# Kernel optimization log

Measured on AMD Instinct MI355X. Metric: run time of the kernel, lower is better.

## Reference

```python
import jax, jax.numpy as jnp
import numpy as np
from jax import lax

K = 16  # knn_k


def _mlp(x, W1, b1, W2, b2):
    h = jax.nn.gelu(x @ W1 + b1, approximate=False)  # torch nn.GELU default = exact
    return h @ W2 + b2


def setup_inputs() -> dict:
    key = jax.random.key(0)
    ks = jax.random.split(key, 10)
    B, N, F, H = 8, 4096, 64, 128

    def xav(k, shape):
        fan_in = shape[0]
        return (jax.random.normal(k, shape, jnp.float32) / np.sqrt(fan_in)).astype(jnp.float32)

    return {
        "coords": jax.random.normal(ks[0], (B, N, 3), jnp.float32),
        "features": jax.random.normal(ks[1], (B, N, F), jnp.float32),
        "inv_W1": xav(ks[2], (6, H)), "inv_b1": jnp.zeros((H,), jnp.float32),
        "inv_W2": xav(ks[3], (H, H)), "inv_b2": jnp.zeros((H,), jnp.float32),
        "feat_W1": xav(ks[4], (F, H)), "feat_b1": jnp.zeros((H,), jnp.float32),
        "feat_W2": xav(ks[5], (H, H)), "feat_b2": jnp.zeros((H,), jnp.float32),
        "sh_W1": xav(ks[6], (2 * H, H)), "sh_b1": jnp.zeros((H,), jnp.float32),
        "sh_W2": xav(ks[7], (H, H)), "sh_b2": jnp.zeros((H,), jnp.float32),
        "g0_W": xav(ks[8], (H, 1)), "g0_b": jnp.zeros((1,), jnp.float32),
    }


def _local_geometry(coords):
    # coords: [B,N,3]
    B, N, _ = coords.shape
    k = min(K, N - 1)
    # squared pairwise distances (monotone in euclidean dist -> same kNN indices)
    sq = jnp.sum(coords * coords, axis=-1)                    # [B,N]
    dist2 = sq[:, :, None] + sq[:, None, :] - 2.0 * jnp.einsum("bnd,bmd->bnm", coords, coords)
    dist2 = lax.stop_gradient(dist2)
    eye = jnp.eye(N, dtype=bool)
    dist2 = jnp.where(eye[None], jnp.inf, dist2)
    _, idx = lax.top_k(-dist2, k)                             # smallest-k -> [B,N,k]
    neighbors = jax.vmap(lambda c, i: c[i])(coords, idx)      # [B,N,k,3]
    relative = neighbors - coords[:, :, None, :]              # [B,N,k,3]
    cov = jnp.einsum("bnki,bnkj->bnij", relative, relative) / float(k)  # [B,N,3,3]
    evals, evecs = jnp.linalg.eigh(cov)                       # ascending
    normals = evecs[..., 0]                                   # smallest-eigval eigenvector, [B,N,3]
    center = coords.mean(axis=1, keepdims=True)
    outward = coords - center
    orient = jnp.sign(jnp.sum(normals * outward, axis=-1, keepdims=True))
    orient = jnp.where(orient == 0, 1.0, orient)
    normals = normals * orient
    normals = normals / jnp.maximum(jnp.linalg.norm(normals, axis=-1, keepdims=True), 1e-6)
    radius = jnp.linalg.norm(relative, axis=-1).mean(axis=-1, keepdims=True)   # [B,N,1]
    centered_radius = jnp.linalg.norm(outward, axis=-1, keepdims=True)
    eig_sum = jnp.maximum(evals.sum(axis=-1, keepdims=True), 1e-6)
    dominance = evals[..., 2:3] / eig_sum
    invariants = jnp.concatenate([evals, radius, centered_radius, dominance], axis=-1)  # [B,N,6]
    return normals, invariants


def reference(coords, features, inv_W1, inv_b1, inv_W2, inv_b2,
              feat_W1, feat_b1, feat_W2, feat_b2,
              sh_W1, sh_b1, sh_W2, sh_b2, g0_W, g0_b):
    normals, invariants = _local_geometry(coords)
    inv_h = _mlp(invariants, inv_W1, inv_b1, inv_W2, inv_b2)
    feat_h = _mlp(features, feat_W1, feat_b1, feat_W2, feat_b2)
    hidden = _mlp(jnp.concatenate([inv_h, feat_h], axis=-1), sh_W1, sh_b1, sh_W2, sh_b2)
    scalar = hidden @ g0_W + g0_b                                   # grade 0, [B,N,1]
    plane = jnp.stack([normals[..., 0], normals[..., 1], -normals[..., 2],
                       -jnp.sum(coords * normals, axis=-1)], axis=-1)  # grade 1, [B,N,4]
    biv = jnp.concatenate([normals, jnp.zeros_like(normals)], axis=-1)  # grade 2, [B,N,6]
    point = jnp.concatenate([coords, jnp.ones(coords.shape[:-1] + (1,), coords.dtype)], axis=-1)  # grade 3 OPNS point
    zero4 = jnp.zeros(coords.shape[:-1] + (1,), coords.dtype)            # grade 4
    return jnp.concatenate([scalar, plane, biv, point, zero4], axis=-1)  # [B,N,16]
```

## Files before the change

kernel.cpp:

```cpp
#include <hip/hip_runtime.h>
#include <hip/hip_bf16.h>

#define BB 8
#define NN 4096
#define FF 64
#define HH 128
#define KNN 16

typedef __attribute__((ext_vector_type(8))) short bf16x8;
typedef __attribute__((ext_vector_type(4))) short bf16x4;
typedef __attribute__((ext_vector_type(4))) float f32x4;

#define OFF_iW2 0
#define OFF_fW1 16384
#define OFF_fW2 24576
#define OFF_sW1 40960
#define OFF_sW2 73728
#define HI_SZ   90112

__device__ __forceinline__ float sq3(float x, float y, float z) {
    return fmaf(z, z, fmaf(y, y, __fmul_rn(x, x)));
}
__device__ __forceinline__ float dist2f(float px, float py, float pz, float psq, float4 cc) {
    float t = fmaf(pz, cc.z, fmaf(py, cc.y, __fmul_rn(px, cc.x)));
    return __fsub_rn(__fadd_rn(psq, cc.w), __fmul_rn(2.0f, t));
}

__device__ __forceinline__ short f2bf(float x) {
    unsigned u = __float_as_uint(x);
    u += 0x7fffu + ((u >> 16) & 1u);
    return (short)(u >> 16);
}
__device__ __forceinline__ float bf2f(short s) {
    return __uint_as_float(((unsigned)(unsigned short)s) << 16);
}

extern "C" __global__ __launch_bounds__(256)
void k_prep(const float* __restrict__ coords, float4* __restrict__ coords4, float* __restrict__ center,
            const float* __restrict__ iW2, const float* __restrict__ fW1,
            const float* __restrict__ fW2, const float* __restrict__ sW1,
            const float* __restrict__ sW2, short* __restrict__ wbf) {
    const int bx = blockIdx.x, tid = threadIdx.x;
    __shared__ float rx[256], ry[256], rz[256];
    if (bx < 8) {
        const int b = bx;
        float sx = 0.f, sy = 0.f, sz = 0.f;
        for (int n = tid; n < NN; n += 256) {
            const float* c = coords + (size_t)(b * NN + n) * 3;
            float x = c[0], y = c[1], z = c[2];
            coords4[b * NN + n] = make_float4(x, y, z, sq3(x, y, z));
            sx += x; sy += y; sz += z;
        }
        rx[tid] = sx; ry[tid] = sy; rz[tid] = sz;
        __syncthreads();
        for (int s = 128; s > 0; s >>= 1) {
            if (tid < s) { rx[tid] += rx[tid + s]; ry[tid] += ry[tid + s]; rz[tid] += rz[tid + s]; }
            __syncthreads();
        }
        if (tid == 0) {
            center[b * 4 + 0] = rx[0] * (1.0f / NN);
            center[b * 4 + 1] = ry[0] * (1.0f / NN);
            center[b * 4 + 2] = rz[0] * (1.0f / NN);
        }
    } else {
        const int wb = bx - 8;
        const int w = wb >> 4;
        const int xb = wb & 15;
        const float* W; int K; int off;
        if (w == 0)      { W = iW2; K = 128; off = OFF_iW2; }
        else if (w == 1) { W = fW1; K = 64;  off = OFF_fW1; }
        else if (w == 2) { W = fW2; K = 128; off = OFF_fW2; }
        else if (w == 3) { W = sW1; K = 256; off = OFF_sW1; }
        else             { W = sW2; K = 128; off = OFF_sW2; }
        short* hi = wbf + off;
        short* lo = wbf + HI_SZ + off;
        const int total = K * 128;
        for (int e = xb * 256 + tid; e < total; e += 4096) {
            int j = e & 7, lane = (e >> 3) & 63, ct = (e >> 9) & 7, kb = e >> 12;
            int k = kb * 32 + (lane >> 4) * 8 + j;
            int n = ct * 16 + (lane & 15);
            float v = W[k * 128 + n];
            short h = f2bf(v);
            float r = v - bf2f(h);
            hi[e] = h; lo[e] = f2bf(r);
        }
    }
}

#define JROT(app, aqq, apq, arp, arq, vp0, vp1, vp2, vq0, vq1, vq2) { \
    float tau_ = (aqq - app) / (2.0f * apq); \
    float tt_ = copysignf(1.0f, tau_) / (fabsf(tau_) + sqrtf(1.0f + tau_ * tau_)); \
    if (apq == 0.0f) tt_ = 0.0f; \
    float cc_ = 1.0f / sqrtf(1.0f + tt_ * tt_); \
    float ss_ = tt_ * cc_; \
    float app_n = cc_*cc_*app - 2.0f*cc_*ss_*apq + ss_*ss_*aqq; \
    float aqq_n = ss_*ss_*app + 2.0f*cc_*ss_*apq + cc_*cc_*aqq; \
    float apq_n = cc_*ss_*(app - aqq) + (cc_*cc_ - ss_*ss_)*apq; \
    float arp_n = cc_*arp - ss_*arq; \
    float arq_n = ss_*arp + cc_*arq; \
    app = app_n; aqq = aqq_n; apq = apq_n; arp = arp_n; arq = arq_n; \
    float t0_ = cc_*vp0 - ss_*vq0, t1_ = cc_*vp1 - ss_*vq1, t2_ = cc_*vp2 - ss_*vq2; \
    vq0 = ss_*vp0 + cc_*vq0; vq1 = ss_*vp1 + cc_*vq1; vq2 = ss_*vp2 + cc_*vq2; \
    vp0 = t0_; vp1 = t1_; vp2 = t2_; }

#define SWAPF(a, b) { float sw_ = a; a = b; b = sw_; }

__device__ __forceinline__ void sort16(float (&d)[16]) {
#pragma unroll
    for (int k = 2; k <= 16; k <<= 1) {
#pragma unroll
        for (int j = k >> 1; j > 0; j >>= 1) {
#pragma unroll
            for (int i = 0; i < 16; i++) {
                int l = i ^ j;
                if (l > i) {
                    if ((i & k) == 0) {
                        float mn = fminf(d[i], d[l]);
                        d[l] = fmaxf(d[i], d[l]);
                        d[i] = mn;
                    } else {
                        float mx = fmaxf(d[i], d[l]);
                        d[l] = fminf(d[i], d[l]);
                        d[i] = mx;
                    }
                }
            }
        }
    }
}

__device__ __forceinline__ void merge16(float (&dk)[16], const float (&d)[16]) {
    float t[16];
#pragma unroll
    for (int i = 0; i < 16; i++) t[i] = fminf(dk[i], d[15 - i]);
#pragma unroll
    for (int j = 8; j > 0; j >>= 1) {
#pragma unroll
        for (int i = 0; i < 16; i++) {
            int l = i ^ j;
            if (l > i) {
                float mn = fminf(t[i], t[l]);
                t[l] = fmaxf(t[i], t[l]);
                t[i] = mn;
            }
        }
    }
#pragma unroll
    for (int i = 0; i < 16; i++) dk[i] = t[i];
}

__device__ __forceinline__ void sort16i(int (&d)[16]) {
#pragma unroll
    for (int k = 2; k <= 16; k <<= 1) {
#pragma unroll
        for (int j = k >> 1; j > 0; j >>= 1) {
#pragma unroll
            for (int i = 0; i < 16; i++) {
                int l = i ^ j;
                if (l > i) {
                    int a = d[i], bq = d[l];
                    int mn = a < bq ? a : bq;
                    int mx = a < bq ? bq : a;
                    if ((i & k) == 0) { d[i] = mn; d[l] = mx; }
                    else              { d[i] = mx; d[l] = mn; }
                }
            }
        }
    }
}

__device__ __forceinline__ float gelu_exact(float x) {
    return 0.5f * x * (1.0f + erff(x * 0.70710678118654752440f));
}

template <int KB, bool INIT>
__device__ __forceinline__ void gemm_mfma(const short* Ab, const short* __restrict__ whi,
                                          const short* __restrict__ wlo,
                                          const float* __restrict__ bias,
                                          int wid, int lane, f32x4 acc[2]) {
    const int m16 = lane & 15, quad = lane >> 4;
    if (INIT) {
        float b0 = bias[wid * 16 + m16];
        acc[0] = (f32x4){b0, b0, b0, b0};
        acc[1] = acc[0];
    }
#pragma unroll 1
    for (int kb = 0; kb < KB; kb++) {
        bf16x8 a0 = *(const bf16x8*)(Ab + m16 * 136 + kb * 32 + quad * 8);
        bf16x8 a1 = *(const bf16x8*)(Ab + (m16 + 16) * 136 + kb * 32 + quad * 8);
        const int off = ((kb * 8 + wid) * 64 + lane) * 8;
        bf16x8 bh = *(const bf16x8*)(whi + off);
        bf16x8 bl = *(const bf16x8*)(wlo + off);
        acc[0] = __builtin_amdgcn_mfma_f32_16x16x32_bf16(a0, bh, acc[0], 0, 0, 0);
        acc[0] = __builtin_amdgcn_mfma_f32_16x16x32_bf16(a0, bl, acc[0], 0, 0, 0);
        acc[1] = __builtin_amdgcn_mfma_f32_16x16x32_bf16(a1, bh, acc[1], 0, 0, 0);
        acc[1] = __builtin_amdgcn_mfma_f32_16x16x32_bf16(a1, bl, acc[1], 0, 0, 0);
    }
}

__device__ __forceinline__ void acc_to_bf(short* dst, f32x4 acc[2], int wid, int lane, bool dogelu) {
    const int m16 = lane & 15, quad = lane >> 4;
#pragma unroll
    for (int mt = 0; mt < 2; mt++)
#pragma unroll
        for (int i = 0; i < 4; i++) {
            float v = acc[mt][i];
            if (dogelu) v = gelu_exact(v);
            dst[(mt * 16 + quad * 4 + i) * 136 + wid * 16 + m16] = f2bf(v);
        }
}

extern "C" __global__ __launch_bounds__(512, 8)
void k_fused(const float4* __restrict__ coords4, const float* __restrict__ center,
             const float* __restrict__ features, const short* __restrict__ wbf,
             const float* __restrict__ iW1, const float* __restrict__ ib1,
             const float* __restrict__ ib2,
             const float* __restrict__ fb1, const float* __restrict__ fb2,
             const float* __restrict__ sb1, const float* __restrict__ sb2,
             const float* __restrict__ gW, const float* __restrict__ gb,
             float* __restrict__ out) {
    const int blk = blockIdx.x;
    const int b = blk >> 7;
    const int chunk = blk & 127;
    const int tid = threadIdx.x;
    const int pid = tid & 31;
    const int h = tid >> 5;
    const int n = chunk * 32 + pid;
    const float4* __restrict__ C = coords4 + b * NN;

    __shared__ __align__(16) char smem[36864];
    float4* tile = (float4*)smem;
    float* mb = (float*)smem;
    unsigned short* slist = (unsigned short*)(smem + 16384);
    unsigned short* tlist = (unsigned short*)(smem + 17408);
    int* cnt_s = (int*)(smem + 17920);
    int* cnt_t = (int*)(smem + 18048);
    float* inv8 = (float*)(smem + 18176);
    float* sc   = (float*)(smem + 19200);
    short* Abf  = (short*)(smem + 19328);
    short* FHbf = (short*)(smem + 28032);

    float4 me = C[n];
    const float px = me.x, py = me.y, pz = me.z, psq = me.w;
    const float INF = __builtin_inff();

    float dk[KNN];
#pragma unroll
    for (int i = 0; i < KNN; i++) dk[i] = INF;

    for (int r = 0; r < 4; r++) {
        __syncthreads();
#pragma unroll
        for (int e = tid; e < 1024; e += 512) {
            int seg = e >> 6, idx = e & 63;
            tile[e] = C[seg * 256 + r * 64 + idx];
        }
        __syncthreads();
        const float4* T = &tile[h * 64];
        const int selfj = n - (h * 256 + r * 64);
#pragma unroll
        for (int bt = 0; bt < 4; bt++) {
            float d[16];
#pragma unroll
            for (int i = 0; i < 16; i++) {
                float4 cc = T[bt * 16 + i];
                float dd = dist2f(px, py, pz, psq, cc);
                d[i] = (bt * 16 + i) == selfj ? INF : dd;
            }
            sort16(d);
            merge16(dk, d);
        }
    }

    {
        float o[16];
#pragma unroll
        for (int i = 0; i < KNN; i++) o[i] = __shfl_xor(dk[i], 32);
        merge16(dk, o);
    }
#pragma unroll
    for (int s = 64; s <= 256; s <<= 1) {
        __syncthreads();
#pragma unroll
        for (int i = 0; i < KNN; i++) mb[tid * 17 + i] = dk[i];
        __syncthreads();
        const int ptn = tid ^ s;
        float o[16];
#pragma unroll
        for (int i = 0; i < KNN; i++) o[i] = mb[ptn * 17 + i];
        merge16(dk, o);
    }
    const float d15 = dk[15];

    __syncthreads();
    if (tid < 32) { cnt_s[tid] = 0; cnt_t[tid] = 0; }

    for (int r = 0; r < 4; r++) {
        __syncthreads();
#pragma unroll
        for (int e = tid; e < 1024; e += 512) {
            int seg = e >> 6, idx = e & 63;
            tile[e] = C[seg * 256 + r * 64 + idx];
        }
        __syncthreads();
        const float4* T = &tile[h * 64];
        const int base = h * 256 + r * 64;
#pragma unroll 4
        for (int j = 0; j < 64; j++) {
            float4 cc = T[j];
            float d = dist2f(px, py, pz, psq, cc);
            int g = base + j;
            if (g != n && d <= d15) {
                if (d < d15) {
                    int pos = atomicAdd(&cnt_s[pid], 1);
                    if (pos < 16) slist[pid * 16 + pos] = (unsigned short)g;
                } else {
                    int pos = atomicAdd(&cnt_t[pid], 1);
                    if (pos < 8) tlist[pid * 8 + pos] = (unsigned short)g;
                }
            }
        }
    }
    __syncthreads();

    if (tid < 32) {
        int ns = cnt_s[tid]; ns = ns > 15 ? 15 : ns;
        int ids[16];
#pragma unroll
        for (int j = 0; j < 16; j++) {
            int tj = j - ns; tj = tj < 0 ? 0 : (tj > 7 ? 7 : tj);
            int sid = (int)slist[tid * 16 + j];
            int tie = (int)tlist[tid * 8 + tj];
            ids[j] = (j < ns) ? sid : tie;
        }
        sort16i(ids);

        float cxx = 0.f, cxy = 0.f, cxz = 0.f, cyy = 0.f, cyz = 0.f, czz = 0.f, radsum = 0.f;
#pragma unroll
        for (int j = 0; j < KNN; j++) {
            float4 cc = C[ids[j]];
            float rx = __fsub_rn(cc.x, px), ry = __fsub_rn(cc.y, py), rz = __fsub_rn(cc.z, pz);
            cxx = __fadd_rn(cxx, __fmul_rn(rx, rx));
            cxy = __fadd_rn(cxy, __fmul_rn(rx, ry));
            cxz = __fadd_rn(cxz, __fmul_rn(rx, rz));
            cyy = __fadd_rn(cyy, __fmul_rn(ry, ry));
            cyz = __fadd_rn(cyz, __fmul_rn(ry, rz));
            czz = __fadd_rn(czz, __fmul_rn(rz, rz));
            float rr = __fadd_rn(__fadd_rn(__fmul_rn(rx, rx), __fmul_rn(ry, ry)), __fmul_rn(rz, rz));
            radsum = __fadd_rn(radsum, sqrtf(rr));
        }
        const float inv_k = 1.0f / KNN;
        float a00 = cxx * inv_k, a01 = cxy * inv_k, a02 = cxz * inv_k;
        float a11 = cyy * inv_k, a12 = cyz * inv_k, a22 = czz * inv_k;

        float V00 = 1.f, V01 = 0.f, V02 = 0.f;
        float V10 = 0.f, V11 = 1.f, V12 = 0.f;
        float V20 = 0.f, V21 = 0.f, V22 = 1.f;
        for (int sweep = 0; sweep < 6; sweep++) {
            JROT(a00, a11, a01, a02, a12, V00, V10, V20, V01, V11, V21);
            JROT(a00, a22, a02, a01, a12, V00, V10, V20, V02, V12, V22);
            JROT(a11, a22, a12, a01, a02, V01, V11, V21, V02, V12, V22);
        }
        float e0 = a00, e1 = a11, e2 = a22;
        float x0 = V00, y0 = V10, z0 = V20;
        float x1 = V01, y1 = V11, z1 = V21;
        float x2 = V02, y2 = V12, z2 = V22;
        if (e0 > e1) { SWAPF(e0, e1); SWAPF(x0, x1); SWAPF(y0, y1); SWAPF(z0, z1); }
        if (e1 > e2) { SWAPF(e1, e2); SWAPF(x1, x2); SWAPF(y1, y2); SWAPF(z1, z2); }
        if (e0 > e1) { SWAPF(e0, e1); SWAPF(x0, x1); SWAPF(y0, y1); SWAPF(z0, z1); }

        float cx = center[b * 4 + 0], cy = center[b * 4 + 1], cz = center[b * 4 + 2];
        float ox = __fsub_rn(px, cx), oy = __fsub_rn(py, cy), oz = __fsub_rn(pz, cz);
        float dt = __fadd_rn(__fadd_rn(__fmul_rn(x0, ox), __fmul_rn(y0, oy)), __fmul_rn(z0, oz));
        float sgn = (dt >= 0.0f) ? 1.0f : -1.0f;
        x0 *= sgn; y0 *= sgn; z0 *= sgn;
        float nrm = sqrtf(__fadd_rn(__fadd_rn(__fmul_rn(x0, x0), __fmul_rn(y0, y0)), __fmul_rn(z0, z0)));
        float den = fmaxf(nrm, 1e-6f);
        x0 = x0 / den; y0 = y0 / den; z0 = z0 / den;

        float radius = radsum * inv_k;
        float crad = sqrtf(__fadd_rn(__fadd_rn(__fmul_rn(ox, ox), __fmul_rn(oy, oy)), __fmul_rn(oz, oz)));
        float esum = fmaxf(__fadd_rn(__fadd_rn(e0, e1), e2), 1e-6f);
        float dom = e2 / esum;

        float* ip = inv8 + tid * 8;
        ip[0] = e0; ip[1] = e1; ip[2] = e2; ip[3] = radius; ip[4] = crad; ip[5] = dom;
        ip[6] = 0.f; ip[7] = 0.f;

        float pd = __fadd_rn(__fadd_rn(__fmul_rn(px, x0), __fmul_rn(py, y0)), __fmul_rn(pz, z0));
        float4* o = (float4*)(out + (size_t)(b * NN + n) * 16);
        o[0] = make_float4(0.0f, x0, y0, -z0);
        o[1] = make_float4(-pd, x0, y0, z0);
        o[2] = make_float4(0.0f, 0.0f, 0.0f, px);
        o[3] = make_float4(py, pz, 1.0f, 0.0f);
        sc[tid] = gb[0];
    }
    __syncthreads();

    const int wid = tid >> 6, lane = tid & 63;
    const short* w_iW2h = wbf + OFF_iW2; const short* w_iW2l = wbf + HI_SZ + OFF_iW2;
    const short* w_fW1h = wbf + OFF_fW1; const short* w_fW1l = wbf + HI_SZ + OFF_fW1;
    const short* w_fW2h = wbf + OFF_fW2; const short* w_fW2l = wbf + HI_SZ + OFF_fW2;
    const short* w_sW1h = wbf + OFF_sW1; const short* w_sW1l = wbf + HI_SZ + OFF_sW1;
    const short* w_sW2h = wbf + OFF_sW2; const short* w_sW2l = wbf + HI_SZ + OFF_sW2;
    f32x4 acc[2];

    {
        int row = tid >> 4, c4 = (tid & 15) * 4;
        const float* s = features + (size_t)(b * NN + chunk * 32 + row) * FF + c4;
        float4 v = *(const float4*)s;
        bf16x4 pk;
        pk[0] = f2bf(v.x); pk[1] = f2bf(v.y); pk[2] = f2bf(v.z); pk[3] = f2bf(v.w);
        *(bf16x4*)(Abf + row * 136 + c4) = pk;
    }
    __syncthreads();

    gemm_mfma<2, true>(Abf, w_fW1h, w_fW1l, fb1, wid, lane, acc);
    __syncthreads();
    acc_to_bf(Abf, acc, wid, lane, true);
    __syncthreads();

    gemm_mfma<4, true>(Abf, w_fW2h, w_fW2l, fb2, wid, lane, acc);
    __syncthreads();
    acc_to_bf(FHbf, acc, wid, lane, false);

    {
        const int cg = tid & 31, pg = tid >> 5;
        const int c0 = cg * 4, p0 = pg * 2;
        float4 bb = *(const float4*)(ib1 + c0);
        float a2[2][4];
#pragma unroll
        for (int i = 0; i < 2; i++) { a2[i][0] = bb.x; a2[i][1] = bb.y; a2[i][2] = bb.z; a2[i][3] = bb.w; }
#pragma unroll
        for (int k = 0; k < 6; k++) {
            float4 w = *(const float4*)(iW1 + k * HH + c0);
#pragma unroll
            for (int i = 0; i < 2; i++) {
                float a = inv8[(p0 + i) * 8 + k];
                a2[i][0] = fmaf(a, w.x, a2[i][0]);
                a2[i][1] = fmaf(a, w.y, a2[i][1]);
                a2[i][2] = fmaf(a, w.z, a2[i][2]);
                a2[i][3] = fmaf(a, w.w, a2[i][3]);
            }
        }
#pragma unroll
        for (int i = 0; i < 2; i++) {
            bf16x4 pk;
            pk[0] = f2bf(gelu_exact(a2[i][0])); pk[1] = f2bf(gelu_exact(a2[i][1]));
            pk[2] = f2bf(gelu_exact(a2[i][2])); pk[3] = f2bf(gelu_exact(a2[i][3]));
            *(bf16x4*)(Abf + (p0 + i) * 136 + c0) = pk;
        }
    }
    __syncthreads();

    gemm_mfma<4, true>(Abf, w_iW2h, w_iW2l, ib2, wid, lane, acc);
    __syncthreads();
    acc_to_bf(Abf, acc, wid, lane, false);
    __syncthreads();

    gemm_mfma<4, true>(Abf, w_sW1h, w_sW1l, sb1, wid, lane, acc);
    gemm_mfma<4, false>(FHbf, w_sW1h + 16384, w_sW1l + 16384, nullptr, wid, lane, acc);
    __syncthreads();
    acc_to_bf(Abf, acc, wid, lane, true);
    __syncthreads();

    gemm_mfma<4, true>(Abf, w_sW2h, w_sW2l, sb2, wid, lane, acc);
    {
        const int m16 = lane & 15, quad = lane >> 4;
        float g = gW[wid * 16 + m16];
#pragma unroll
        for (int mt = 0; mt < 2; mt++)
#pragma unroll
            for (int i = 0; i < 4; i++)
                atomicAdd(&sc[mt * 16 + quad * 4 + i], acc[mt][i] * g);
    }
    __syncthreads();
    if (tid < 32) out[(size_t)(b * NN + chunk * 32 + tid) * 16] = sc[tid];
}

extern "C" void kernel_launch(void* const* d_in, const int* in_sizes, int n_in,
                              void* d_out, int out_size, void* d_ws, size_t ws_size,
                              hipStream_t stream) {
    const float* coords   = (const float*)d_in[0];
    const float* features = (const float*)d_in[1];
    const float* iW1 = (const float*)d_in[2],  * ib1 = (const float*)d_in[3];
    const float* iW2 = (const float*)d_in[4],  * ib2 = (const float*)d_in[5];
    const float* fW1 = (const float*)d_in[6],  * fb1 = (const float*)d_in[7];
    const float* fW2 = (const float*)d_in[8],  * fb2 = (const float*)d_in[9];
    const float* sW1 = (const float*)d_in[10], * sb1 = (const float*)d_in[11];
    const float* sW2 = (const float*)d_in[12], * sb2 = (const float*)d_in[13];
    const float* gW  = (const float*)d_in[14], * gb  = (const float*)d_in[15];
    float* out = (float*)d_out;

    float* ws = (float*)d_ws;
    float4* coords4 = (float4*)ws;
    float* center = ws + BB * NN * 4;
    short* wbf = (short*)((char*)d_ws + 524416);

    hipLaunchKernelGGL(k_prep, dim3(88), dim3(256), 0, stream,
                       coords, coords4, center, iW2, fW1, fW2, sW1, sW2, wbf);
    hipLaunchKernelGGL(k_fused, dim3(1024), dim3(512), 0, stream, coords4, center, features, wbf,
                       iW1, ib1, ib2, fb1, fb2, sb1, sb2, gW, gb, out);
}
```

Measured before the change: 265.7 us.

## Interleave kNN candidate split across lanes, reduce with shuffles, read coords from global

Each point's 16 helper threads now sit in adjacent lanes within a wavefront and take candidates in interleaved order (j*16+h). The cross-thread top-k reduction is then four xor-shuffle merges instead of a cross-wave shared-memory exchange with barriers. Coordinate tiles are no longer staged in LDS; candidates are read directly from global/L2, which shrinks shared memory and removes the per-round barriers. The bitonic sort16 is replaced by an explicit 63-comparator merge-sort network, and merge16 now works in place. The cost is that global coordinate loads now rely on the cache rather than LDS reuse.

```diff
diff --git a/kernel.cpp b/kernel.cpp
--- a/kernel.cpp
+++ b/kernel.cpp
@@ -105,48 +105,49 @@
 
 #define SWAPF(a, b) { float sw_ = a; a = b; b = sw_; }
 
+__device__ __forceinline__ void ce(float& a, float& b) {
+    float mn = fminf(a, b);
+    b = fmaxf(a, b);
+    a = mn;
+}
+
 __device__ __forceinline__ void sort16(float (&d)[16]) {
-#pragma unroll
-    for (int k = 2; k <= 16; k <<= 1) {
-#pragma unroll
-        for (int j = k >> 1; j > 0; j >>= 1) {
-#pragma unroll
-            for (int i = 0; i < 16; i++) {
-                int l = i ^ j;
-                if (l > i) {
-                    if ((i & k) == 0) {
-                        float mn = fminf(d[i], d[l]);
-                        d[l] = fmaxf(d[i], d[l]);
-                        d[i] = mn;
-                    } else {
-                        float mx = fmaxf(d[i], d[l]);
-                        d[l] = fminf(d[i], d[l]);
-                        d[i] = mx;
-                    }
-                }
-            }
-        }
-    }
-}
-
-__device__ __forceinline__ void merge16(float (&dk)[16], const float (&d)[16]) {
-    float t[16];
-#pragma unroll
-    for (int i = 0; i < 16; i++) t[i] = fminf(dk[i], d[15 - i]);
-#pragma unroll
-    for (int j = 8; j > 0; j >>= 1) {
+    ce(d[0],d[1]); ce(d[2],d[3]); ce(d[0],d[2]); ce(d[1],d[3]); ce(d[1],d[2]);
+    ce(d[4],d[5]); ce(d[6],d[7]); ce(d[4],d[6]); ce(d[5],d[7]); ce(d[5],d[6]);
+    ce(d[0],d[4]); ce(d[2],d[6]); ce(d[2],d[4]);
+    ce(d[1],d[5]); ce(d[3],d[7]); ce(d[3],d[5]);
+    ce(d[1],d[2]); ce(d[3],d[4]); ce(d[5],d[6]);
+    ce(d[8],d[9]); ce(d[10],d[11]); ce(d[8],d[10]); ce(d[9],d[11]); ce(d[9],d[10]);
+    ce(d[12],d[13]); ce(d[14],d[15]); ce(d[12],d[14]); ce(d[13],d[15]); ce(d[13],d[14]);
+    ce(d[8],d[12]); ce(d[10],d[14]); ce(d[10],d[12]);
+    ce(d[9],d[13]); ce(d[11],d[15]); ce(d[11],d[13]);
+    ce(d[9],d[10]); ce(d[11],d[12]); ce(d[13],d[14]);
+    ce(d[0],d[8]); ce(d[4],d[12]); ce(d[4],d[8]);
+    ce(d[2],d[10]); ce(d[6],d[14]); ce(d[6],d[10]);
+    ce(d[2],d[4]); ce(d[6],d[8]); ce(d[10],d[12]);
+    ce(d[1],d[9]); ce(d[5],d[13]); ce(d[5],d[9]);
+    ce(d[3],d[11]); ce(d[7],d[15]); ce(d[7],d[11]);
+    ce(d[3],d[5]); ce(d[7],d[9]); ce(d[11],d[13]);
+    ce(d[1],d[2]); ce(d[3],d[4]); ce(d[5],d[6]); ce(d[7],d[8]);
+    ce(d[9],d[10]); ce(d[11],d[12]); ce(d[13],d[14]);
+}
+
+__device__ __forceinline__ void merge16(float (&dk)[16], float (&d)[16]) {
+#pragma unroll
+    for (int i = 0; i < 8; i++) {
+        float a  = fminf(dk[i], d[15 - i]);
+        float b2 = fminf(dk[15 - i], d[i]);
+        d[i] = a; d[15 - i] = b2;
+    }
+#pragma unroll
+    for (int j = 8; j > 0; j >>= 1)
 #pragma unroll
         for (int i = 0; i < 16; i++) {
             int l = i ^ j;
-            if (l > i) {
-                float mn = fminf(t[i], t[l]);
-                t[l] = fmaxf(t[i], t[l]);
-                t[i] = mn;
-            }
-        }
-    }
-#pragma unroll
-    for (int i = 0; i < 16; i++) dk[i] = t[i];
+            if (l > i) ce(d[i], d[l]);
+        }
+#pragma unroll
+    for (int i = 0; i < 16; i++) dk[i] = d[i];
 }
 
 __device__ __forceinline__ void sort16i(int (&d)[16]) {
@@ -223,107 +224,74 @@
     const int b = blk >> 7;
     const int chunk = blk & 127;
     const int tid = threadIdx.x;
-    const int pid = tid & 31;
-    const int h = tid >> 5;
+    const int h = tid & 15;
+    const int pid = tid >> 4;
     const int n = chunk * 32 + pid;
     const float4* __restrict__ C = coords4 + b * NN;
 
-    __shared__ __align__(16) char smem[36864];
-    float4* tile = (float4*)smem;
-    float* mb = (float*)smem;
-    unsigned short* slist = (unsigned short*)(smem + 16384);
-    unsigned short* tlist = (unsigned short*)(smem + 17408);
-    int* cnt_s = (int*)(smem + 17920);
-    int* cnt_t = (int*)(smem + 18048);
-    float* inv8 = (float*)(smem + 18176);
-    float* sc   = (float*)(smem + 19200);
-    short* Abf  = (short*)(smem + 19328);
-    short* FHbf = (short*)(smem + 28032);
+    __shared__ __align__(16) char smem[20352];
+    unsigned short* slist = (unsigned short*)(smem);
+    unsigned short* tlist = (unsigned short*)(smem + 1024);
+    int* cnt_s = (int*)(smem + 1536);
+    int* cnt_t = (int*)(smem + 1664);
+    float* inv8 = (float*)(smem + 1792);
+    float* sc   = (float*)(smem + 2816);
+    short* Abf  = (short*)(smem + 2944);
+    short* FHbf = (short*)(smem + 11648);
+
+    if (tid < 32) { cnt_s[tid] = 0; cnt_t[tid] = 0; }
 
     float4 me = C[n];
     const float px = me.x, py = me.y, pz = me.z, psq = me.w;
     const float INF = __builtin_inff();
+    const int self_j = ((n & 15) == h) ? (n >> 4) : 256;
 
     float dk[KNN];
 #pragma unroll
     for (int i = 0; i < KNN; i++) dk[i] = INF;
 
-    for (int r = 0; r < 4; r++) {
-        __syncthreads();
-#pragma unroll
-        for (int e = tid; e < 1024; e += 512) {
-            int seg = e >> 6, idx = e & 63;
-            tile[e] = C[seg * 256 + r * 64 + idx];
-        }
-        __syncthreads();
-        const float4* T = &tile[h * 64];
-        const int selfj = n - (h * 256 + r * 64);
-#pragma unroll
-        for (int bt = 0; bt < 4; bt++) {
-            float d[16];
-#pragma unroll
-            for (int i = 0; i < 16; i++) {
-                float4 cc = T[bt * 16 + i];
-                float dd = dist2f(px, py, pz, psq, cc);
-                d[i] = (bt * 16 + i) == selfj ? INF : dd;
+    for (int bt = 0; bt < 16; bt++) {
+        float d[16];
+#pragma unroll
+        for (int i = 0; i < 16; i++) {
+            float4 cc = C[(bt * 16 + i) * 16 + h];
+            float dd = dist2f(px, py, pz, psq, cc);
+            d[i] = (bt * 16 + i) == self_j ? INF : dd;
+        }
+        sort16(d);
+        merge16(dk, d);
+    }
+
+#pragma unroll
+    for (int m = 1; m <= 8; m <<= 1) {
+        float o[16];
+#pragma unroll
+        for (int i = 0; i < KNN; i++) o[i] = __shfl_xor(dk[i], m);
+        merge16(dk, o);
+    }
+    const float d15 = dk[15];
+
+    __syncthreads();
+
+#pragma unroll 4
+    for (int j = 0; j < 256; j++) {
+        float4 cc = C[j * 16 + h];
+        float d = dist2f(px, py, pz, psq, cc);
+        if (j != self_j && d <= d15) {
+            if (d < d15) {
+                int pos = atomicAdd(&cnt_s[pid], 1);
+                if (pos < 16) slist[pid * 16 + pos] = (unsigned short)(j * 16 + h);
+            } else {
+                int pos = atomicAdd(&cnt_t[pid], 1);
+                if (pos < 8) tlist[pid * 8 + pos] = (unsigned short)(j * 16 + h);
             }
-            sort16(d);
-            merge16(dk, d);
-        }
-    }
-
-    {
-        float o[16];
-#pragma unroll
-        for (int i = 0; i < KNN; i++) o[i] = __shfl_xor(dk[i], 32);
-        merge16(dk, o);
-    }
-#pragma unroll
-    for (int s = 64; s <= 256; s <<= 1) {
-        __syncthreads();
-#pragma unroll
-        for (int i = 0; i < KNN; i++) mb[tid * 17 + i] = dk[i];
-        __syncthreads();
-        const int ptn = tid ^ s;
-        float o[16];
-#pragma unroll
-        for (int i = 0; i < KNN; i++) o[i] = mb[ptn * 17 + i];
-        merge16(dk, o);
-    }
-    const float d15 = dk[15];
-
-    __syncthreads();
-    if (tid < 32) { cnt_s[tid] = 0; cnt_t[tid] = 0; }
-
-    for (int r = 0; r < 4; r++) {
-        __syncthreads();
-#pragma unroll
-        for (int e = tid; e < 1024; e += 512) {
-            int seg = e >> 6, idx = e & 63;
-            tile[e] = C[seg * 256 + r * 64 + idx];
-        }
-        __syncthreads();
-        const float4* T = &tile[h * 64];
-        const int base = h * 256 + r * 64;
-#pragma unroll 4
-        for (int j = 0; j < 64; j++) {
-            float4 cc = T[j];
-            float d = dist2f(px, py, pz, psq, cc);
-            int g = base + j;
-            if (g != n && d <= d15) {
-                if (d < d15) {
-                    int pos = atomicAdd(&cnt_s[pid], 1);
-                    if (pos < 16) slist[pid * 16 + pos] = (unsigned short)g;
-                } else {
-                    int pos = atomicAdd(&cnt_t[pid], 1);
-                    if (pos < 8) tlist[pid * 8 + pos] = (unsigned short)g;
-                }
-            }
         }
     }
     __syncthreads();
 
     if (tid < 32) {
+        const int np = chunk * 32 + tid;
+        float4 pme = C[np];
         int ns = cnt_s[tid]; ns = ns > 15 ? 15 : ns;
         int ids[16];
 #pragma unroll
@@ -339,7 +307,7 @@
 #pragma unroll
         for (int j = 0; j < KNN; j++) {
             float4 cc = C[ids[j]];
-            float rx = __fsub_rn(cc.x, px), ry = __fsub_rn(cc.y, py), rz = __fsub_rn(cc.z, pz);
+            float rx = __fsub_rn(cc.x, pme.x), ry = __fsub_rn(cc.y, pme.y), rz = __fsub_rn(cc.z, pme.z);
             cxx = __fadd_rn(cxx, __fmul_rn(rx, rx));
             cxy = __fadd_rn(cxy, __fmul_rn(rx, ry));
             cxz = __fadd_rn(cxz, __fmul_rn(rx, rz));
@@ -370,7 +338,7 @@
         if (e0 > e1) { SWAPF(e0, e1); SWAPF(x0, x1); SWAPF(y0, y1); SWAPF(z0, z1); }
 
         float cx = center[b * 4 + 0], cy = center[b * 4 + 1], cz = center[b * 4 + 2];
-        float ox = __fsub_rn(px, cx), oy = __fsub_rn(py, cy), oz = __fsub_rn(pz, cz);
+        float ox = __fsub_rn(pme.x, cx), oy = __fsub_rn(pme.y, cy), oz = __fsub_rn(pme.z, cz);
         float dt = __fadd_rn(__fadd_rn(__fmul_rn(x0, ox), __fmul_rn(y0, oy)), __fmul_rn(z0, oz));
         float sgn = (dt >= 0.0f) ? 1.0f : -1.0f;
         x0 *= sgn; y0 *= sgn; z0 *= sgn;
@@ -387,12 +355,12 @@
         ip[0] = e0; ip[1] = e1; ip[2] = e2; ip[3] = radius; ip[4] = crad; ip[5] = dom;
         ip[6] = 0.f; ip[7] = 0.f;
 
-        float pd = __fadd_rn(__fadd_rn(__fmul_rn(px, x0), __fmul_rn(py, y0)), __fmul_rn(pz, z0));
-        float4* o = (float4*)(out + (size_t)(b * NN + n) * 16);
+        float pd = __fadd_rn(__fadd_rn(__fmul_rn(pme.x, x0), __fmul_rn(pme.y, y0)), __fmul_rn(pme.z, z0));
+        float4* o = (float4*)(out + (size_t)(b * NN + np) * 16);
         o[0] = make_float4(0.0f, x0, y0, -z0);
         o[1] = make_float4(-pd, x0, y0, z0);
-        o[2] = make_float4(0.0f, 0.0f, 0.0f, px);
-        o[3] = make_float4(py, pz, 1.0f, 0.0f);
+        o[2] = make_float4(0.0f, 0.0f, 0.0f, pme.x);
+        o[3] = make_float4(pme.y, pme.z, 1.0f, 0.0f);
         sc[tid] = gb[0];
     }
     __syncthreads();
```

Result: slower. 295.9 us (+11.4%).
